# Kernel optimization log

Measured on AMD Instinct MI355X. Metric: run time of the kernel, lower is better.

The kernel has to match this reference:

```python
import jax, jax.numpy as jnp
import numpy as np

B, L, DK, DV = 16, 8192, 128, 128
ALPHA, LR, BETA = 0.02, 0.1, 0.9
SCALE = 0.05  # keeps lr*||k||^2 small -> stable delta-rule recurrence


def setup_inputs() -> dict:
    key = jax.random.key(0)
    kq, kk, kv = jax.random.split(key, 3)
    Q = jax.random.normal(kq, (B, L, DK), dtype=jnp.float32) * SCALE
    K = jax.random.normal(kk, (B, L, DK), dtype=jnp.float32) * SCALE
    V = jax.random.normal(kv, (B, L, DV), dtype=jnp.float32) * SCALE
    return {"Q": Q, "K": K, "V": V}


def reference(Q, K, V):
    # TitansMemory: reset -> per-step update_step(k_t, v_t) -> read(q_t).
    # W_t = (1-alpha) W_{t-1} - lr * m_t,  m_t = beta m_{t-1} + (1-beta) grad_t
    # grad_t = 2 (W_{t-1} k_t - v_t) k_t^T ;  y_t = W_t q_t
    b, l, dk = K.shape
    dv = V.shape[-1]
    W0 = jnp.zeros((b, dv, dk), dtype=K.dtype)
    m0 = jnp.zeros_like(W0)

    def step(carry, inp):
        W, m = carry
        k, v, q = inp  # [B,dk], [B,dv], [B,dk]
        resid = jnp.einsum('bvk,bk->bv', W, k) - v          # Wk - v
        grad = 2.0 * resid[:, :, None] * k[:, None, :]       # [B,dv,dk]
        m = BETA * m + (1.0 - BETA) * grad
        W = (1.0 - ALPHA) * W - LR * m
        y = jnp.einsum('bvk,bk->bv', W, q)                   # read with updated W
        return (W, m), y

    xs = (jnp.swapaxes(K, 0, 1), jnp.swapaxes(V, 0, 1), jnp.swapaxes(Q, 0, 1))
    (_, _), Y = jax.lax.scan(step, (W0, m0), xs)             # Y: [L,B,dv]
    return jnp.swapaxes(Y, 0, 1)                              # [B,L,dv]
```

## Files before the change

kernel.cpp:

```cpp
#include <hip/hip_runtime.h>


#define L_ 8192
#define D_ 128

typedef __attribute__((ext_vector_type(4))) float f4;
typedef __attribute__((ext_vector_type(2))) unsigned int u2;

constexpr float A_    = 0.98f;
constexpr float BETA_ = 0.9f;
constexpr float C_S   = -0.02f;

template <int CTRL>
__device__ __forceinline__ float dpp_add(float x) {
  int y = __builtin_amdgcn_update_dpp(0, __float_as_int(x), CTRL, 0xF, 0xF, true);
  return x + __int_as_float(y);
}

__device__ __forceinline__ float half_sum_all(float x) {
  x = dpp_add<0x121>(x);
  x = dpp_add<0x122>(x);
  x = dpp_add<0x124>(x);
  x = dpp_add<0x128>(x);
  u2 p = __builtin_amdgcn_permlane16_swap(__float_as_uint(x), __float_as_uint(x),
                                          false, false);
  return __uint_as_float(p.x) + __uint_as_float(p.y);
}

#define GLD4(dst, addr, OFF) \
  asm volatile("global_load_dwordx4 %0, %1, off offset:" OFF : "=v"(dst) : "v"(addr))
#define GLD1(dst, addr, OFF) \
  asm volatile("global_load_dword %0, %1, off offset:" OFF : "=v"(dst) : "v"(addr))

#define ISSUE_CHUNK(kb, qb, vb)                            \
  do {                                                     \
    GLD4(kb[0], ka64, "0");    GLD4(qb[0], qa64, "0");    GLD1(vb[0], va64, "0");    \
    GLD4(kb[1], ka64, "512");  GLD4(qb[1], qa64, "512");  GLD1(vb[1], va64, "512");  \
    GLD4(kb[2], ka64, "1024"); GLD4(qb[2], qa64, "1024"); GLD1(vb[2], va64, "1024"); \
    GLD4(kb[3], ka64, "1536"); GLD4(qb[3], qa64, "1536"); GLD1(vb[3], va64, "1536"); \
    GLD4(kb[4], ka64, "2048"); GLD4(qb[4], qa64, "2048"); GLD1(vb[4], va64, "2048"); \
    GLD4(kb[5], ka64, "2560"); GLD4(qb[5], qa64, "2560"); GLD1(vb[5], va64, "2560"); \
    GLD4(kb[6], ka64, "3072"); GLD4(qb[6], qa64, "3072"); GLD1(vb[6], va64, "3072"); \
    GLD4(kb[7], ka64, "3584"); GLD4(qb[7], qa64, "3584"); GLD1(vb[7], va64, "3584"); \
    uint64_t bump_ = (sc < 1023) ? 4096u : 0u;             \
    ka64 += bump_; qa64 += bump_; va64 += bump_; ++sc;     \
  } while (0)

#define WAITP                                              \
  do {                                                     \
    asm volatile("s_waitcnt vmcnt(24)");                   \
    __builtin_amdgcn_sched_barrier(0);                     \
  } while (0)

__global__ __launch_bounds__(64, 1)
void TitansMemory_188978561365_kernel(const float* __restrict__ Q,
                                      const float* __restrict__ K,
                                      const float* __restrict__ V,
                                      float* __restrict__ Y) {
  const int lane  = threadIdx.x;
  const int wid   = blockIdx.x;
  const int batch = wid >> 6;
  const int row   = ((wid & 63) << 1) | (lane >> 5);
  const int col   = (lane & 31) << 2;

  const size_t bbase = (size_t)batch * (size_t)L_ * D_;
  uint64_t ka64 = (uint64_t)(K + bbase + col);
  uint64_t qa64 = (uint64_t)(Q + bbase + col);
  uint64_t va64 = (uint64_t)(V + bbase + row);
  float*   yst  = Y + bbase + row + (size_t)(lane & 31) * D_;
  int sc = 0;

  const f4 av = {A_, A_, A_, A_};
  const f4 bv = {BETA_, BETA_, BETA_, BETA_};

  f4 w = {0.f, 0.f, 0.f, 0.f}, m = {0.f, 0.f, 0.f, 0.f};
  float yl = 0.f;

  f4 kA[8], qA[8]; float vA[8];
  f4 kB[8], qB[8]; float vB[8];

  auto step = [&](const f4& k, const f4& q, float v, int j32) {
    f4 d = w * k;
    float dot = half_sum_all((d.x + d.y) + (d.z + d.w));
    float s = fmaf(C_S, dot, (-C_S) * v);
    f4 s4 = {s, s, s, s};
    m = __builtin_elementwise_fma(s4, k, bv * m);
    w = __builtin_elementwise_fma(av, w, m);
    f4 e = w * q;
    float y = half_sum_all((e.x + e.y) + (e.z + e.w));
    yl = ((lane & 31) == j32) ? y : yl;
  };

  ISSUE_CHUNK(kA, qA, vA);
  ISSUE_CHUNK(kB, qB, vB);

  for (int it = 0; it < L_ / 32; ++it) {
    WAITP;
#pragma unroll
    for (int j = 0; j < 8; ++j) step(kA[j], qA[j], vA[j], j);
    ISSUE_CHUNK(kA, qA, vA);
    WAITP;
#pragma unroll
    for (int j = 0; j < 8; ++j) step(kB[j], qB[j], vB[j], 8 + j);
    ISSUE_CHUNK(kB, qB, vB);
    WAITP;
#pragma unroll
    for (int j = 0; j < 8; ++j) step(kA[j], qA[j], vA[j], 16 + j);
    ISSUE_CHUNK(kA, qA, vA);
    WAITP;
#pragma unroll
    for (int j = 0; j < 8; ++j) step(kB[j], qB[j], vB[j], 24 + j);
    ISSUE_CHUNK(kB, qB, vB);
    *yst = yl;
    yst += 32 * D_;
  }
}

extern "C" void kernel_launch(void* const* d_in, const int* in_sizes, int n_in,
                              void* d_out, int out_size, void* d_ws, size_t ws_size,
                              hipStream_t stream) {
  const float* Q = (const float*)d_in[0];
  const float* K = (const float*)d_in[1];
  const float* V = (const float*)d_in[2];
  float* Y = (float*)d_out;
  dim3 grid(1024), block(64);
  hipLaunchKernelGGL(TitansMemory_188978561365_kernel, grid, block, 0, stream,
                     Q, K, V, Y);
}
```

Before: 1.098 ms.

## Defer output reductions out of the recurrence and batch them with permlane swaps

The cross-lane reduction for each output y is removed from the per-step critical path. Each step now only produces a per-lane partial dot product. Every 8 steps, the partials are combined in pairs via permlane16_swap and a DPP reduction, then written by one lane per 16-lane group. This takes the second full reduction off the serial dependency chain and replaces the select-based accumulation with batched reductions. In exchange it adds extra stores of fewer values and some reduction work off the critical path.

New measurement: 1.190 ms. 1.08x slower.

```diff
diff --git a/kernel.cpp b/kernel.cpp
--- a/kernel.cpp
+++ b/kernel.cpp
@@ -5,6 +5,7 @@
 #define D_ 128
 
 typedef __attribute__((ext_vector_type(4))) float f4;
+typedef __attribute__((ext_vector_type(2))) float f2;
 typedef __attribute__((ext_vector_type(2))) unsigned int u2;
 
 constexpr float A_    = 0.98f;
@@ -60,35 +61,52 @@
   const int lane  = threadIdx.x;
   const int wid   = blockIdx.x;
   const int batch = wid >> 6;
-  const int row   = ((wid & 63) << 1) | (lane >> 5);
   const int col   = (lane & 31) << 2;
 
   const size_t bbase = (size_t)batch * (size_t)L_ * D_;
   uint64_t ka64 = (uint64_t)(K + bbase + col);
   uint64_t qa64 = (uint64_t)(Q + bbase + col);
-  uint64_t va64 = (uint64_t)(V + bbase + row);
-  float*   yst  = Y + bbase + row + (size_t)(lane & 31) * D_;
+  uint64_t va64 = (uint64_t)(V + bbase + ((wid & 63) << 1) + (lane >> 5));
+  float* yb = Y + bbase + ((wid & 63) << 1) + (lane >> 5)
+                + (size_t)((lane >> 4) & 1) * D_;
   int sc = 0;
 
   const f4 av = {A_, A_, A_, A_};
   const f4 bv = {BETA_, BETA_, BETA_, BETA_};
 
   f4 w = {0.f, 0.f, 0.f, 0.f}, m = {0.f, 0.f, 0.f, 0.f};
-  float yl = 0.f;
 
   f4 kA[8], qA[8]; float vA[8];
   f4 kB[8], qB[8]; float vB[8];
+  float ey[8];
 
-  auto step = [&](const f4& k, const f4& q, float v, int j32) {
+  auto step = [&](const f4& k, const f4& q, float v) -> float {
     f4 d = w * k;
-    float dot = half_sum_all((d.x + d.y) + (d.z + d.w));
+    f2 dp = {d.x + d.z, d.y + d.w};
+    float dot = half_sum_all(dp.x + dp.y);
     float s = fmaf(C_S, dot, (-C_S) * v);
     f4 s4 = {s, s, s, s};
     m = __builtin_elementwise_fma(s4, k, bv * m);
     w = __builtin_elementwise_fma(av, w, m);
     f4 e = w * q;
-    float y = half_sum_all((e.x + e.y) + (e.z + e.w));
-    yl = ((lane & 31) == j32) ? y : yl;
+    f2 ep = {e.x + e.z, e.y + e.w};
+    return ep.x + ep.y;
+  };
+
+  auto flushY = [&]() {
+#pragma unroll
+    for (int p = 0; p < 4; ++p) {
+      u2 r = __builtin_amdgcn_permlane16_swap(__float_as_uint(ey[2 * p]),
+                                              __float_as_uint(ey[2 * p + 1]),
+                                              false, false);
+      float c = __uint_as_float(r.x) + __uint_as_float(r.y);
+      c = dpp_add<0x121>(c);
+      c = dpp_add<0x122>(c);
+      c = dpp_add<0x124>(c);
+      c = dpp_add<0x128>(c);
+      if ((lane & 15) == 0) yb[(size_t)(2 * p) * D_] = c;
+    }
+    yb += 8 * D_;
   };
 
   ISSUE_CHUNK(kA, qA, vA);
@@ -97,22 +115,24 @@
   for (int it = 0; it < L_ / 32; ++it) {
     WAITP;
 #pragma unroll
-    for (int j = 0; j < 8; ++j) step(kA[j], qA[j], vA[j], j);
+    for (int j = 0; j < 8; ++j) ey[j] = step(kA[j], qA[j], vA[j]);
+    flushY();
     ISSUE_CHUNK(kA, qA, vA);
     WAITP;
 #pragma unroll
-    for (int j = 0; j < 8; ++j) step(kB[j], qB[j], vB[j], 8 + j);
+    for (int j = 0; j < 8; ++j) ey[j] = step(kB[j], qB[j], vB[j]);
+    flushY();
     ISSUE_CHUNK(kB, qB, vB);
     WAITP;
 #pragma unroll
-    for (int j = 0; j < 8; ++j) step(kA[j], qA[j], vA[j], 16 + j);
+    for (int j = 0; j < 8; ++j) ey[j] = step(kA[j], qA[j], vA[j]);
+    flushY();
     ISSUE_CHUNK(kA, qA, vA);
     WAITP;
 #pragma unroll
-    for (int j = 0; j < 8; ++j) step(kB[j], qB[j], vB[j], 24 + j);
+    for (int j = 0; j < 8; ++j) ey[j] = step(kB[j], qB[j], vB[j]);
+    flushY();
     ISSUE_CHUNK(kB, qB, vB);
-    *yst = yl;
-    yst += 32 * D_;
   }
 }
 
```
